# Optimization experiments

Measured on AMD Instinct MI355X. Metric: run time of the kernel, lower is better.

## Reference

```python
import jax, jax.numpy as jnp
import numpy as np
import functools

N, D, R, E, L, C, MAXDEG = 40000, 128, 3, 640000, 2, 40, 512
BN_EPS = 1e-5


def setup_inputs():
    ks = iter(jax.random.split(jax.random.key(0), 40))
    nrm = lambda s, sc=0.05: jax.random.normal(next(ks), s, dtype=jnp.float32) * sc
    x = jax.random.normal(next(ks), (N, D), dtype=jnp.float32)
    edge_indices = jax.random.randint(next(ks), (R, 2, E), 0, N, dtype=jnp.int32)
    out_emb = nrm((L, MAXDEG, D)).at[:, 0].set(0.0)  # padding_idx=0 -> zero row
    in_emb = nrm((L, MAXDEG, D)).at[:, 0].set(0.0)
    return dict(
        x=x, edge_indices=edge_indices,
        W_src=nrm((L, D, D)), b_src=nrm((L, D)),
        W_dst=nrm((L, D, D)), b_dst=nrm((L, D)),
        W_outf=nrm((L, D)), b_outf=nrm((L,)),
        W_inf=nrm((L, D)), b_inf=nrm((L,)),
        W_fc=nrm((L, D, D)), b_fc=nrm((L, D)),
        bn_gamma=jnp.ones((L, D), jnp.float32), bn_beta=jnp.zeros((L, D), jnp.float32),
        out_deg_emb=out_emb, in_deg_emb=in_emb,
        out_mask=jnp.ones((R, N), jnp.float32), out_mask_bias=jnp.zeros((R, N), jnp.float32),
        in_mask=jnp.ones((R, N), jnp.float32), in_mask_bias=jnp.zeros((R, N), jnp.float32),
        alpha=jnp.float32(0.5), tau=jnp.float32(0.0),
        W_lin=nrm((D, C)), b_lin=nrm((C,)),
    )


def _forward(x, W_src, b_src, W_dst, b_dst, W_outf, b_outf, W_inf, b_inf,
             W_fc, b_fc, bn_gamma, bn_beta, out_deg_emb, in_deg_emb,
             out_mask, out_mask_bias, in_mask, in_mask_bias, alpha, tau,
             W_lin, b_lin, edge_indices):
    seg = lambda d, i: jax.ops.segment_sum(d, i, num_segments=N)
    # source builds I with arange(0, N-1): identity with last diagonal entry missing
    i_mask = (jnp.arange(N) < N - 1).astype(jnp.float32)[:, None]

    rel = []
    for r in range(R):
        row, col = edge_indices[r, 0], edge_indices[r, 1]
        ones = jnp.ones(E, jnp.float32)
        out_deg, in_deg = seg(ones, row), seg(ones, col)
        ods = jnp.where(out_deg > 0, 1.0 / jnp.sqrt(jnp.maximum(out_deg, 1.0)), 0.0)
        ids_ = jnp.where(in_deg > 0, 1.0 / jnp.sqrt(jnp.maximum(in_deg, 1.0)), 0.0)
        # 'dir' norm: D_out^{-1/2} A D_in^{-1/2}; the transposed adj shares the same edge weights
        w = ods[row] * ids_[col]
        rel.append((row, col, w,
                    jnp.clip(out_deg, 0, MAXDEG - 1).astype(jnp.int32),
                    jnp.clip(in_deg, 0, MAXDEG - 1).astype(jnp.int32)))

    def spmm(r_, y):  # adj_norm @ y : gather cols, scatter-add to rows
        row, col, w = rel[r_][0], rel[r_][1], rel[r_][2]
        return seg(w[:, None] * y[col], row)

    def spmm_t(r_, y):  # adj_norm^T @ y
        row, col, w = rel[r_][0], rel[r_][1], rel[r_][2]
        return seg(w[:, None] * y[row], col)

    def dirichlet(mm, y):
        x1 = y / (jnp.sum(jnp.abs(y), axis=1, keepdims=True) + 1e-12)  # row_l1_normalize
        x1sq = x1 * x1
        return (i_mask * x1sq + mm(x1sq)) - 2.0 * ((i_mask * x1 + mm(x1)) * x1 - x1sq)

    eff_tau = jnp.exp(tau) + 0.1

    def conv(l, h):
        out = jnp.zeros((N, D), h.dtype)
        cis, cos_ = [], []
        for r in range(R):
            mm = functools.partial(spmm, r)
            mmt = functools.partial(spmm_t, r)
            out_nei, in_nei = mm(h), mmt(h)
            e_out, e_in = dirichlet(mm, h), dirichlet(mmt, h)
            c_out = (-e_out + out_deg_emb[l][rel[r][3]]) @ W_outf[l] + b_outf[l]  # [N]
            c_in = (-e_in + in_deg_emb[l][rel[r][4]]) @ W_inf[l] + b_inf[l]
            cm = jax.nn.softmax(jnp.stack([c_out, c_in], axis=1) / eff_tau, axis=1)  # tau_softmax
            c_out = cm[:, 0] * out_mask[r] + out_mask_bias[r]
            c_in = cm[:, 1] * in_mask[r] + in_mask_bias[r]
            out = out + c_out[:, None] * (out_nei @ W_src[l] + b_src[l]) \
                      + c_in[:, None] * (in_nei @ W_dst[l] + b_dst[l])
            cis.append(c_in)
            cos_.append(c_out)
        out = out / R
        # F.pad(x,(0,dim-x.shape[1])) is a no-op since input_dim == output_dim
        output = out + alpha * (h @ W_fc[l] + b_fc[l])
        mu, var = jnp.mean(output, axis=0), jnp.var(output, axis=0)  # BatchNorm1d (train mode)
        output = (output - mu) / jnp.sqrt(var + BN_EPS) * bn_gamma[l] + bn_beta[l]
        return output, jnp.mean(jnp.stack(cis), 0)[:, None], jnp.mean(jnp.stack(cos_), 0)[:, None]

    pos_h, neg_h = x, x
    pos_hs, neg_hs, gs, cins, couts = [], [], [], [], []
    for l in range(L):
        ph, ci, co = conv(l, pos_h)
        ph = jax.nn.relu(ph)  # jumping_knowledge truthy -> relu every layer; dropout p=0
        perm = jax.random.permutation(jax.random.key(100 + l), N)  # torch.randperm
        nh, _, _ = conv(l, neg_h[perm])
        nh = jax.nn.relu(nh)
        pos_h, neg_h = ph, nh
        pos_hs.append(ph)
        neg_hs.append(nh)
        gs.append(jnp.mean(ph, axis=0, keepdims=True))
        cins.append(ci)
        couts.append(co)
    c_ins = jnp.mean(jnp.stack(cins), 0)
    c_outs = jnp.mean(jnp.stack(couts), 0)
    jk = functools.reduce(jnp.maximum, pos_hs)  # JumpingKnowledge mode='max'
    logp = jax.nn.log_softmax(jk @ W_lin + b_lin, axis=1)
    return (logp, c_ins, c_outs, *pos_hs, *neg_hs, *gs)


def reference(x, edge_indices, W_src, b_src, W_dst, b_dst, W_outf, b_outf,
              W_inf, b_inf, W_fc, b_fc, bn_gamma, bn_beta, out_deg_emb,
              in_deg_emb, out_mask, out_mask_bias, in_mask, in_mask_bias,
              alpha, tau, W_lin, b_lin):
    return _forward(x, W_src, b_src, W_dst, b_dst, W_outf, b_outf, W_inf, b_inf,
                    W_fc, b_fc, bn_gamma, bn_beta, out_deg_emb, in_deg_emb,
                    out_mask, out_mask_bias, in_mask, in_mask_bias, alpha, tau,
                    W_lin, b_lin, edge_indices)
```

## Files before the change

### kernel.cpp

```cpp
#include <hip/hip_runtime.h>

constexpr int Nn = 40000;
constexpr int Dd = 128;
constexpr int Rr = 3;
constexpr int Ee = 640000;
constexpr int Ll = 2;
constexpr int Cc = 40;
constexpr int MAXD = 512;
constexpr float BN_EPS = 1e-5f;

constexpr int RB_ELEMS = 1024;
constexpr int RB_NB = (Nn + RB_ELEMS - 1) / RB_ELEMS;
constexpr int RB_BINS = 256;

constexpr int EB_ELEMS = 4096;
constexpr int EB_NB = (Ee + EB_ELEMS - 1) / EB_ELEMS;
constexpr int EB_H = 256 * EB_NB;

constexpr int HR_BINS = 13334;
constexpr int HR_PAD = 13344;
constexpr int HR_SB = 16;
constexpr int HR_CHUNK = (Ee + HR_SB - 1) / HR_SB;

__device__ __forceinline__ unsigned rotl32(unsigned x, int d) { return (x << d) | (x >> (32 - d)); }

__device__ void threefry2x32(unsigned k0, unsigned k1, unsigned c0, unsigned c1,
                             unsigned& o0, unsigned& o1) {
  unsigned ks2 = k0 ^ k1 ^ 0x1BD11BDAu;
  unsigned x0 = c0 + k0, x1 = c1 + k1;
#define TFR4(a,b,c,d2) \
  x0 += x1; x1 = rotl32(x1,a);  x1 ^= x0; \
  x0 += x1; x1 = rotl32(x1,b);  x1 ^= x0; \
  x0 += x1; x1 = rotl32(x1,c);  x1 ^= x0; \
  x0 += x1; x1 = rotl32(x1,d2); x1 ^= x0;
  TFR4(13,15,26,6);  x0 += k1;  x1 += ks2 + 1u;
  TFR4(17,29,16,24); x0 += ks2; x1 += k0 + 2u;
  TFR4(13,15,26,6);  x0 += k0;  x1 += k1 + 3u;
  TFR4(17,29,16,24); x0 += k1;  x1 += ks2 + 4u;
  TFR4(13,15,26,6);  x0 += ks2; x1 += k0 + 5u;
#undef TFR4
  o0 = x0; o1 = x1;
}

__global__ void k_genkeys(unsigned* __restrict__ keys, unsigned seed, int rounds,
                          int* __restrict__ vout, int doIota) {
  int i = blockIdx.x * blockDim.x + threadIdx.x;
  if (i >= Nn) return;
  unsigned k0 = 0u, k1 = seed, sk0 = 0u, sk1 = 0u;
  for (int rd = 0; rd < rounds; rd++) {
    unsigned a0, a1, b0, b1;
    threefry2x32(k0, k1, 0u, 0u, a0, a1);
    threefry2x32(k0, k1, 0u, 1u, b0, b1);
    sk0 = b0; sk1 = b1;
    k0 = a0; k1 = a1;
  }
  unsigned o0, o1;
  threefry2x32(sk0, sk1, 0u, (unsigned)i, o0, o1);
  keys[i] = o0 ^ o1;
  if (doIota) vout[i] = i;
}

__global__ void k_rhist(const unsigned* __restrict__ keys, int* __restrict__ hist, int shift) {
  __shared__ int lh[RB_BINS];
  int t = threadIdx.x;
  lh[t] = 0;
  __syncthreads();
  int base = blockIdx.x * RB_ELEMS;
  for (int i = t; i < RB_ELEMS; i += 256) {
    int g = base + i;
    if (g < Nn) atomicAdd(&lh[(keys[g] >> shift) & 255], 1);
  }
  __syncthreads();
  hist[t * RB_NB + blockIdx.x] = lh[t];
}

__device__ void scan_body(const int* cnt, int* off, int n, int items) {
  int t = threadIdx.x;
  int lo = t * items, hi = min(lo + items, n);
  int s = 0;
  for (int i = lo; i < hi; i++) s += cnt[i];
  int lane = t & 63, wid = t >> 6;
  int sc = s;
#pragma unroll
  for (int o = 1; o < 64; o <<= 1) {
    int v = __shfl_up(sc, o);
    if (lane >= o) sc += v;
  }
  __shared__ int wsum[16], woff[16];
  if (lane == 63) wsum[wid] = sc;
  __syncthreads();
  if (t == 0) {
    int a = 0;
    for (int w = 0; w < 16; w++) { woff[w] = a; a += wsum[w]; }
    off[n] = a;
  }
  __syncthreads();
  int run = woff[wid] + sc - s;
  for (int i = lo; i < hi; i++) {
    int v = cnt[i];
    off[i] = run;
    run += v;
  }
}

__global__ __launch_bounds__(1024) void k_scanN(const int* __restrict__ cnt, int* __restrict__ off,
                                                int n, int items) {
  scan_body(cnt, off, n, items);
}

__global__ __launch_bounds__(1024) void k_scan6(const int* __restrict__ odeg, const int* __restrict__ ideg,
                                                int* __restrict__ csr_off, int* __restrict__ csc_off) {
  int b = blockIdx.x;
  const int* cnt = (b < 3) ? (odeg + b * Nn) : (ideg + (b - 3) * Nn);
  int* off = (b < 3) ? (csr_off + b * (Nn + 1)) : (csc_off + (b - 3) * (Nn + 1));
  scan_body(cnt, off, Nn, (Nn + 1023) / 1024);
}

__global__ void k_rscatter(const unsigned* __restrict__ keys, const int* __restrict__ vals,
                           const int* __restrict__ scanned, int shift,
                           unsigned* __restrict__ okeys, int* __restrict__ ovals) {
  __shared__ int running[RB_BINS];
  __shared__ int wcount[4][RB_BINS];
  __shared__ int dbase[RB_BINS];
  int t = threadIdx.x;
  int lane = t & 63, w = t >> 6;
  running[t] = 0;
  dbase[t] = scanned[t * RB_NB + blockIdx.x];
  int base = blockIdx.x * RB_ELEMS;
  for (int rnd = 0; rnd < 4; rnd++) {
#pragma unroll
    for (int q = 0; q < 4; q++) wcount[q][t] = 0;
    __syncthreads();
    int g = base + rnd * 256 + t;
    bool valid = g < Nn;
    unsigned key = valid ? keys[g] : 0u;
    int d = (key >> shift) & 255;
    unsigned long long bb = __ballot(valid);
    unsigned long long mask = bb;
#pragma unroll
    for (int k = 0; k < 8; k++) {
      bool b = (d >> k) & 1;
      unsigned long long tt = __ballot(b && valid);
      mask &= b ? tt : ~tt;
    }
    mask &= bb;
    int riw = __popcll(mask & ((1ull << lane) - 1ull));
    int cnt_ = __popcll(mask);
    if (valid && riw == 0) wcount[w][d] = cnt_;
    __syncthreads();
    if (valid) {
      int prior = 0;
#pragma unroll
      for (int ww = 0; ww < 4; ww++) if (ww < w) prior += wcount[ww][d];
      int gp = dbase[d] + running[d] + prior + riw;
      okeys[gp] = key;
      ovals[gp] = vals[g];
    }
    __syncthreads();
    running[t] += wcount[0][t] + wcount[1][t] + wcount[2][t] + wcount[3][t];
    __syncthreads();
  }
}

__global__ void k_permrows(const float* __restrict__ src, const int* __restrict__ perm,
                           float* __restrict__ dst) {
  int row = blockIdx.x * 8 + (threadIdx.x >> 5);
  int lane = threadIdx.x & 31;
  if (row >= Nn) return;
  int p = perm[row];
  ((float4*)(dst + (size_t)row * Dd))[lane] = ((const float4*)(src + (size_t)p * Dd))[lane];
}

__global__ __launch_bounds__(256) void k_hist2(const int* __restrict__ ei, int* __restrict__ partials) {
  __shared__ int lh[HR_BINS];
  int bid = blockIdx.x;
  int sb = bid % HR_SB;
  int range = (bid / HR_SB) % 3;
  int j = bid / (3 * HR_SB);
  int rel = j >> 1, which = j & 1;
  const int* src = ei + (size_t)rel * 2 * Ee + (size_t)which * Ee;
  int lo = range * HR_BINS;
  for (int i = threadIdx.x; i < HR_BINS; i += 256) lh[i] = 0;
  __syncthreads();
  int e0 = sb * HR_CHUNK, e1 = min(e0 + HR_CHUNK, Ee);
  for (int e = e0 + threadIdx.x; e < e1; e += 256) {
    int v = src[e] - lo;
    if (v >= 0 && v < HR_BINS) atomicAdd(&lh[v], 1);
  }
  __syncthreads();
  int* dst = partials + (size_t)bid * HR_PAD;
  for (int i = threadIdx.x; i < HR_BINS; i += 256) dst[i] = lh[i];
}

__global__ void k_hreduce(const int* __restrict__ partials, int* __restrict__ odeg,
                          int* __restrict__ ideg) {
  int idx = blockIdx.x * 256 + threadIdx.x;
  if (idx >= 6 * Nn) return;
  int j = idx / Nn, bin = idx - j * Nn;
  int range = bin / HR_BINS, off = bin - range * HR_BINS;
  const int* p = partials + (size_t)((j * 3 + range) * HR_SB) * HR_PAD + off;
  int sum = 0;
#pragma unroll
  for (int b = 0; b < HR_SB; b++) sum += p[(size_t)b * HR_PAD];
  int rel = j >> 1;
  (j & 1 ? ideg : odeg)[rel * Nn + bin] = sum;
}

__global__ void k_degnorm(const int* __restrict__ odeg, const int* __restrict__ ideg,
                          float* __restrict__ ods, float* __restrict__ ids,
                          int* __restrict__ odix, int* __restrict__ idix) {
  int idx = blockIdx.x * blockDim.x + threadIdx.x;
  if (idx >= Rr * Nn) return;
  int od = odeg[idx], id_ = ideg[idx];
  ods[idx] = od > 0 ? 1.0f / sqrtf((float)od) : 0.0f;
  ids[idx] = id_ > 0 ? 1.0f / sqrtf((float)id_) : 0.0f;
  odix[idx] = od < MAXD - 1 ? od : MAXD - 1;
  idix[idx] = id_ < MAXD - 1 ? id_ : MAXD - 1;
}

__global__ void k_pack(const int* __restrict__ ei, unsigned* __restrict__ pcsr,
                       unsigned* __restrict__ pcsc) {
  int idx = blockIdx.x * 256 + threadIdx.x;
  if (idx >= 3 * Ee) return;
  int r = idx / Ee, e = idx - r * Ee;
  const int* base = ei + (size_t)r * 2 * Ee;
  unsigned rw = (unsigned)base[e], cl = (unsigned)base[Ee + e];
  pcsr[idx] = (rw << 16) | cl;
  pcsc[idx] = (cl << 16) | rw;
}

__global__ __launch_bounds__(256) void k_ehist(const unsigned* __restrict__ pin,
                                               int* __restrict__ hist, int shift) {
  __shared__ int lh[256];
  int a = blockIdx.x / EB_NB, blk = blockIdx.x % EB_NB;
  const unsigned* src = pin + (size_t)a * Ee;
  lh[threadIdx.x] = 0;
  __syncthreads();
  int base = blk * EB_ELEMS;
  for (int i = threadIdx.x; i < EB_ELEMS; i += 256) {
    int g = base + i;
    if (g < Ee) atomicAdd(&lh[(src[g] >> shift) & 255], 1);
  }
  __syncthreads();
  hist[(size_t)a * EB_H + threadIdx.x * EB_NB + blk] = lh[threadIdx.x];
}

__global__ __launch_bounds__(1024) void k_escan6(const int* __restrict__ hist, int* __restrict__ esc) {
  int a = blockIdx.x;
  scan_body(hist + (size_t)a * EB_H, esc + (size_t)a * (EB_H + 1), EB_H, (EB_H + 1023) / 1024);
}

__global__ __launch_bounds__(256) void k_escatter(const unsigned* __restrict__ pin,
                                                  const int* __restrict__ esc, int shift,
                                                  unsigned* __restrict__ pout) {
  __shared__ int running[256];
  __shared__ int wcount[4][256];
  __shared__ int dbase[256];
  int a = blockIdx.x / EB_NB, blk = blockIdx.x % EB_NB;
  const unsigned* src = pin + (size_t)a * Ee;
  unsigned* dst = pout + (size_t)a * Ee;
  int t = threadIdx.x;
  int lane = t & 63, w = t >> 6;
  running[t] = 0;
  dbase[t] = esc[(size_t)a * (EB_H + 1) + t * EB_NB + blk];
  int base = blk * EB_ELEMS;
  for (int rnd = 0; rnd < 16; rnd++) {
#pragma unroll
    for (int q = 0; q < 4; q++) wcount[q][t] = 0;
    __syncthreads();
    int g = base + rnd * 256 + t;
    bool valid = g < Ee;
    unsigned key = valid ? src[g] : 0u;
    int d = (key >> shift) & 255;
    unsigned long long bb = __ballot(valid);
    unsigned long long mask = bb;
#pragma unroll
    for (int k = 0; k < 8; k++) {
      bool b = (d >> k) & 1;
      unsigned long long tt = __ballot(b && valid);
      mask &= b ? tt : ~tt;
    }
    mask &= bb;
    int riw = __popcll(mask & ((1ull << lane) - 1ull));
    int cnt_ = __popcll(mask);
    if (valid && riw == 0) wcount[w][d] = cnt_;
    __syncthreads();
    if (valid) {
      int prior = 0;
#pragma unroll
      for (int ww = 0; ww < 4; ww++) if (ww < w) prior += wcount[ww][d];
      int gp = dbase[d] + running[d] + prior + riw;
      dst[gp] = key;
    }
    __syncthreads();
    running[t] += wcount[0][t] + wcount[1][t] + wcount[2][t] + wcount[3][t];
    __syncthreads();
  }
}

__global__ void k_rowscalar(const float* __restrict__ h, const float* __restrict__ Wfo,
                            const float* __restrict__ Wfi, float4* __restrict__ aux) {
  int wid = (blockIdx.x * blockDim.x + threadIdx.x) >> 6;
  int lane = threadIdx.x & 63;
  if (wid >= Nn) return;
  float2 a = ((const float2*)(h + (size_t)wid * Dd))[lane];
  float2 wo = ((const float2*)Wfo)[lane];
  float2 wi = ((const float2*)Wfi)[lane];
  float l1 = fabsf(a.x) + fabsf(a.y);
  float so = a.x * a.x * wo.x + a.y * a.y * wo.y;
  float si = a.x * a.x * wi.x + a.y * a.y * wi.y;
#pragma unroll
  for (int o = 32; o; o >>= 1) {
    l1 += __shfl_xor(l1, o);
    so += __shfl_xor(so, o);
    si += __shfl_xor(si, o);
  }
  if (lane == 0) {
    float ri = 1.0f / (l1 + 1e-12f);
    aux[wid] = make_float4(ri, ri * ri * so, ri * ri * si, 0.f);
  }
}

__global__ void k_lut(const float* __restrict__ eo, const float* __restrict__ ei_,
                      const float* __restrict__ Wfo, const float* __restrict__ Wfi,
                      float* __restrict__ luto, float* __restrict__ luti) {
  int wid = (blockIdx.x * blockDim.x + threadIdx.x) >> 6;
  int lane = threadIdx.x & 63;
  if (wid >= MAXD) return;
  float2 a = ((const float2*)(eo + (size_t)wid * Dd))[lane];
  float2 b = ((const float2*)(ei_ + (size_t)wid * Dd))[lane];
  float2 wo = ((const float2*)Wfo)[lane];
  float2 wi = ((const float2*)Wfi)[lane];
  float so = a.x * wo.x + a.y * wo.y;
  float si = b.x * wi.x + b.y * wi.y;
#pragma unroll
  for (int o = 32; o; o >>= 1) { so += __shfl_xor(so, o); si += __shfl_xor(si, o); }
  if (lane == 0) { luto[wid] = so; luti[wid] = si; }
}

__global__ __launch_bounds__(512) void k_csrdir3(
    const int* __restrict__ csr_off, const unsigned* __restrict__ pcsr,
    const int* __restrict__ csc_off, const unsigned* __restrict__ pcsc,
    const float* __restrict__ ods_r, const float* __restrict__ ids_r,
    const float4* __restrict__ aux, const float* __restrict__ h,
    const float* __restrict__ Wfo, const float* __restrict__ Wfi,
    const float* __restrict__ luto, const float* __restrict__ luti,
    const int* __restrict__ odix, const int* __restrict__ idix,
    const float* __restrict__ bo, const float* __restrict__ bi,
    const float* __restrict__ taup,
    const float* __restrict__ omask, const float* __restrict__ omaskb,
    const float* __restrict__ imask, const float* __restrict__ imaskb,
    float* __restrict__ Tout, float* __restrict__ Tin,
    float* __restrict__ sco, float* __restrict__ sci,
    float* __restrict__ co_acc, float* __restrict__ ci_acc,
    int first, int is_pos) {
  __shared__ float lq[8], lp[8], lc[8];
  int t = threadIdx.x;
  int wv = t >> 6, lane = t & 63;
  int dir = wv >> 2;
  int n = blockIdx.x * 4 + (wv & 3);
  const int* off = dir ? csc_off : csr_off;
  const unsigned* nbrp = dir ? pcsc : pcsr;
  const float* scn = dir ? ods_r : ids_r;
  float a_self = (dir ? ids_r : ods_r)[n];
  const float* Wf = dir ? Wfi : Wfo;
  int s0 = off[n], s1 = off[n + 1];
  int hl = lane & 31, half = lane >> 5;
  float4 wf4 = ((const float4*)Wf)[hl];
  float4 hn4 = ((const float4*)(h + (size_t)n * Dd))[hl];
  float rn = aux[n].x;
  float4 s = make_float4(0.f, 0.f, 0.f, 0.f);
  float4 pa = make_float4(0.f, 0.f, 0.f, 0.f);
  float qacc = 0.f;
  for (int base = s0; base < s1; base += 64) {
    int eidx = base + lane;
    bool valid = eidx < s1;
    int mi = valid ? (int)(nbrp[eidx] & 0xFFFFu) : 0;
    float4 av = valid ? aux[mi] : make_float4(0.f, 0.f, 0.f, 0.f);
    float scv = valid ? scn[mi] : 0.f;
    float qsel = dir ? av.z : av.y;
    int cnt = min(64, s1 - base);
#pragma unroll 4
    for (int j = half; j < cnt; j += 2) {
      int m = __shfl(mi, j);
      float sc = __shfl(scv, j);
      float rm = __shfl(av.x, j);
      float qv = __shfl(qsel, j);
      float w = a_self * sc;
      float wrm = w * rm;
      float4 hv = ((const float4*)(h + (size_t)m * Dd))[hl];
      s.x += w * hv.x; s.y += w * hv.y; s.z += w * hv.z; s.w += w * hv.w;
      pa.x += wrm * hv.x; pa.y += wrm * hv.y; pa.z += wrm * hv.z; pa.w += wrm * hv.w;
      qacc += w * qv;
    }
  }
  s.x += __shfl_xor(s.x, 32); s.y += __shfl_xor(s.y, 32);
  s.z += __shfl_xor(s.z, 32); s.w += __shfl_xor(s.w, 32);
  pa.x += __shfl_xor(pa.x, 32); pa.y += __shfl_xor(pa.y, 32);
  pa.z += __shfl_xor(pa.z, 32); pa.w += __shfl_xor(pa.w, 32);
  qacc += __shfl_xor(qacc, 32);
  float pd = rn * (hn4.x * wf4.x * pa.x + hn4.y * wf4.y * pa.y +
                   hn4.z * wf4.z * pa.z + hn4.w * wf4.w * pa.w);
#pragma unroll
  for (int o = 16; o; o >>= 1) pd += __shfl_xor(pd, o);
  if (lane == 0) { lq[wv] = qacc; lp[wv] = pd; }
  __syncthreads();
  if (t < 4) {
    int nn = blockIdx.x * 4 + t;
    float Qo_ = lq[t], Po_ = lp[t], Qi_ = lq[4 + t], Pi_ = lp[4 + t];
    float4 a2 = aux[nn];
    float im = (nn < Nn - 1) ? 1.0f : 0.0f;
    float so_ = luto[odix[nn]] + bo[0] - (Qo_ - 2.0f * Po_ + (2.0f - im) * a2.y);
    float si_ = luti[idix[nn]] + bi[0] - (Qi_ - 2.0f * Pi_ + (2.0f - im) * a2.z);
    float tt = expf(taup[0]) + 0.1f;
    float aa = so_ / tt, bb = si_ / tt;
    float mm = fmaxf(aa, bb);
    float ea = expf(aa - mm), eb = expf(bb - mm);
    float inv = 1.0f / (ea + eb);
    float co = ea * inv * omask[nn] + omaskb[nn];
    float ci = eb * inv * imask[nn] + imaskb[nn];
    lc[t] = co; lc[4 + t] = ci;
    if (first) { sco[nn] = co; sci[nn] = ci; }
    else       { sco[nn] += co; sci[nn] += ci; }
    if (is_pos) { co_acc[nn] += co; ci_acc[nn] += ci; }
  }
  __syncthreads();
  float c = lc[wv];
  if (lane < 32) {
    float* T = dir ? Tin : Tout;
    size_t o = (size_t)n * Dd;
    float4 v = make_float4(c * s.x, c * s.y, c * s.z, c * s.w);
    if (!first) {
      float4 old = ((const float4*)(T + o))[hl];
      v.x += old.x; v.y += old.y; v.z += old.z; v.w += old.w;
    }
    ((float4*)(T + o))[hl] = v;
  }
}

__global__ __launch_bounds__(256) void k_gemmconv(
    const float* __restrict__ Tout, const float* __restrict__ Tin, const float* __restrict__ h,
    const float* __restrict__ Wsrc, const float* __restrict__ Wdst, const float* __restrict__ Wfc,
    const float* __restrict__ bsrc, const float* __restrict__ bdst, const float* __restrict__ bfc,
    const float* __restrict__ sco, const float* __restrict__ sci,
    const float* __restrict__ alphap, float* __restrict__ pre, float* __restrict__ bnsum) {
  __shared__ float Asm[64][36];
  __shared__ float Bsm[32][132];
  __shared__ float lsum[128], lsum2[128];
  int t = threadIdx.x;
  int rg = t >> 5, cg = t & 31;
  int m0 = blockIdx.x * 64;
  int arow = t >> 2, aq = t & 3;
  float alpha = alphap[0];
  float acc[8][4];
#pragma unroll
  for (int r = 0; r < 8; r++)
#pragma unroll
    for (int c = 0; c < 4; c++) acc[r][c] = 0.f;
  for (int kt = 0; kt < 12; kt++) {
    int sec = kt >> 2, kc = (kt & 3) * 32;
    const float* Ap = sec == 0 ? Tout : (sec == 1 ? Tin : h);
    const float* Wp = sec == 0 ? Wsrc : (sec == 1 ? Wdst : Wfc);
    float sA = (sec == 2) ? alpha : (1.0f / (float)Rr);
    __syncthreads();
    {
      const float4* src = (const float4*)(Ap + (size_t)(m0 + arow) * Dd + kc + aq * 8);
      float4 v0 = src[0], v1 = src[1];
      float4* d0 = (float4*)&Asm[arow][aq * 8];
      d0[0] = make_float4(v0.x * sA, v0.y * sA, v0.z * sA, v0.w * sA);
      d0[1] = make_float4(v1.x * sA, v1.y * sA, v1.z * sA, v1.w * sA);
    }
#pragma unroll
    for (int j = 0; j < 4; j++) {
      int idx = t + j * 256;
      int k = idx >> 5, d4 = idx & 31;
      *(float4*)&Bsm[k][d4 * 4] = *(const float4*)(Wp + (size_t)(kc + k) * Dd + d4 * 4);
    }
    __syncthreads();
#pragma unroll
    for (int kk = 0; kk < 32; kk += 4) {
      float4 af[8], bf[4];
#pragma unroll
      for (int r = 0; r < 8; r++) af[r] = *(const float4*)&Asm[rg * 8 + r][kk];
#pragma unroll
      for (int j = 0; j < 4; j++) bf[j] = *(const float4*)&Bsm[kk + j][cg * 4];
#pragma unroll
      for (int r = 0; r < 8; r++) {
        const float* ap = (const float*)&af[r];
#pragma unroll
        for (int j = 0; j < 4; j++) {
          const float* bp = (const float*)&bf[j];
          acc[r][0] += ap[j] * bp[0];
          acc[r][1] += ap[j] * bp[1];
          acc[r][2] += ap[j] * bp[2];
          acc[r][3] += ap[j] * bp[3];
        }
      }
    }
  }
  float4 vb1 = *(const float4*)(bsrc + cg * 4);
  float4 vb2 = *(const float4*)(bdst + cg * 4);
  float4 vbf = *(const float4*)(bfc + cg * 4);
  float ps[4] = {0.f, 0.f, 0.f, 0.f}, ps2[4] = {0.f, 0.f, 0.f, 0.f};
#pragma unroll
  for (int r = 0; r < 8; r++) {
    int row = m0 + rg * 8 + r;
    size_t o = (size_t)row * Dd + cg * 4;
    float s1 = sco[row] * (1.0f / (float)Rr), s2 = sci[row] * (1.0f / (float)Rr);
    float4 v;
    v.x = acc[r][0] + s1 * vb1.x + s2 * vb2.x + alpha * vbf.x;
    v.y = acc[r][1] + s1 * vb1.y + s2 * vb2.y + alpha * vbf.y;
    v.z = acc[r][2] + s1 * vb1.z + s2 * vb2.z + alpha * vbf.z;
    v.w = acc[r][3] + s1 * vb1.w + s2 * vb2.w + alpha * vbf.w;
    *(float4*)(pre + o) = v;
    ps[0] += v.x; ps[1] += v.y; ps[2] += v.z; ps[3] += v.w;
    ps2[0] += v.x * v.x; ps2[1] += v.y * v.y; ps2[2] += v.z * v.z; ps2[3] += v.w * v.w;
  }
  if (t < 128) { lsum[t] = 0.f; lsum2[t] = 0.f; }
  __syncthreads();
#pragma unroll
  for (int j = 0; j < 4; j++) {
    atomicAdd(&lsum[cg * 4 + j], ps[j]);
    atomicAdd(&lsum2[cg * 4 + j], ps2[j]);
  }
  __syncthreads();
  if (t < 128) atomicAdd(&bnsum[t], lsum[t]);
  else if (t < 256) atomicAdd(&bnsum[t], lsum2[t - 128]);
}

__global__ void k_bnapply(const float* __restrict__ pre, const float* __restrict__ sums,
                          const float* __restrict__ gamma, const float* __restrict__ beta,
                          float* __restrict__ hout, float* __restrict__ gs, int do_gs) {
  __shared__ float ls[256];
  int c = threadIdx.x & 127, sub = threadIdx.x >> 7;
  float mu = sums[c] * (1.0f / (float)Nn);
  float var = sums[c + 128] * (1.0f / (float)Nn) - mu * mu;
  float sc = gamma[c] / sqrtf(var + BN_EPS);
  float bt = beta[c];
  float g = 0.f;
  for (int n = blockIdx.x * 2 + sub; n < Nn; n += gridDim.x * 2) {
    float v = (pre[(size_t)n * Dd + c] - mu) * sc + bt;
    v = fmaxf(v, 0.f);
    hout[(size_t)n * Dd + c] = v;
    g += v;
  }
  if (do_gs) {
    ls[threadIdx.x] = g;
    __syncthreads();
    if (sub == 0) atomicAdd(&gs[c], (ls[c] + ls[c + 128]) * (1.0f / (float)Nn));
  }
}

__global__ void k_cio(const float* __restrict__ ci_acc, const float* __restrict__ co_acc,
                      float* __restrict__ cins, float* __restrict__ couts) {
  int n = blockIdx.x * blockDim.x + threadIdx.x;
  if (n < Nn) {
    cins[n] = ci_acc[n] * (1.0f / (float)(Ll * Rr));
    couts[n] = co_acc[n] * (1.0f / (float)(Ll * Rr));
  }
}

__global__ __launch_bounds__(64) void k_logp(const float* __restrict__ ph0, const float* __restrict__ ph1,
                      const float* __restrict__ Wlin, const float* __restrict__ blin,
                      float* __restrict__ logp) {
  __shared__ float jk[Dd];
  __shared__ float lg[Cc];
  int n = blockIdx.x, t = threadIdx.x;
  for (int d = t; d < Dd; d += 64) jk[d] = fmaxf(ph0[(size_t)n * Dd + d], ph1[(size_t)n * Dd + d]);
  __syncthreads();
  if (t < Cc) {
    float acc = blin[t];
    for (int k = 0; k < Dd; k++) acc += jk[k] * Wlin[k * Cc + t];
    lg[t] = acc;
  }
  __syncthreads();
  float m = -1e30f;
  for (int c = 0; c < Cc; c++) m = fmaxf(m, lg[c]);
  float s = 0.f;
  for (int c = 0; c < Cc; c++) s += expf(lg[c] - m);
  float lse = m + logf(s);
  if (t < Cc) logp[(size_t)n * Cc + t] = lg[t] - lse;
}

extern "C" void kernel_launch(void* const* d_in, const int* in_sizes, int n_in,
                              void* d_out, int out_size, void* d_ws, size_t ws_size,
                              hipStream_t stream) {
  const float* x      = (const float*)d_in[0];
  const int*   ei     = (const int*)d_in[1];
  const float* W_src  = (const float*)d_in[2];
  const float* b_src  = (const float*)d_in[3];
  const float* W_dst  = (const float*)d_in[4];
  const float* b_dst  = (const float*)d_in[5];
  const float* W_outf = (const float*)d_in[6];
  const float* b_outf = (const float*)d_in[7];
  const float* W_inf  = (const float*)d_in[8];
  const float* b_inf  = (const float*)d_in[9];
  const float* W_fc   = (const float*)d_in[10];
  const float* b_fc   = (const float*)d_in[11];
  const float* gamma  = (const float*)d_in[12];
  const float* beta   = (const float*)d_in[13];
  const float* oemb   = (const float*)d_in[14];
  const float* iemb   = (const float*)d_in[15];
  const float* omask  = (const float*)d_in[16];
  const float* omaskb = (const float*)d_in[17];
  const float* imask  = (const float*)d_in[18];
  const float* imaskb = (const float*)d_in[19];
  const float* alphap = (const float*)d_in[20];
  const float* taup   = (const float*)d_in[21];
  const float* Wlin   = (const float*)d_in[22];
  const float* blin   = (const float*)d_in[23];

  float* out   = (float*)d_out;
  float* logp  = out;
  float* cins  = logp + (size_t)Nn * Cc;
  float* couts = cins + Nn;
  float* ph0   = couts + Nn;
  float* ph1   = ph0 + (size_t)Nn * Dd;
  float* nh0   = ph1 + (size_t)Nn * Dd;
  float* nh1   = nh0 + (size_t)Nn * Dd;
  float* gs0   = nh1 + (size_t)Nn * Dd;
  float* gs1   = gs0 + Dd;

  char* p = (char*)d_ws;
  auto alloc = [&](size_t bytes) -> void* {
    void* q = (void*)p;
    p += (bytes + 255) & ~(size_t)255;
    return q;
  };
  float* pre   = (float*)alloc((size_t)Nn * Dd * 4);
  float* Tout  = (float*)alloc((size_t)Nn * Dd * 4);
  float* Tin   = (float*)alloc((size_t)Nn * Dd * 4);
  float* hperm = (float*)alloc((size_t)Nn * Dd * 4);
  unsigned* pbuf = (unsigned*)alloc((size_t)6 * Ee * 4);
  size_t qwords = (size_t)6 * Ee;
  size_t pwords = (size_t)(6 * 3 * HR_SB) * HR_PAD;
  unsigned* qbuf = (unsigned*)alloc((qwords > pwords ? qwords : pwords) * 4);
  int* partials = (int*)qbuf;
  int* csr_off = (int*)alloc((size_t)Rr * (Nn + 1) * 4);
  int* csc_off = (int*)alloc((size_t)Rr * (Nn + 1) * 4);
  int* odeg    = (int*)alloc((size_t)Rr * Nn * 4);
  int* ideg    = (int*)alloc((size_t)Rr * Nn * 4);
  float* ods   = (float*)alloc((size_t)Rr * Nn * 4);
  float* ids   = (float*)alloc((size_t)Rr * Nn * 4);
  int* odix    = (int*)alloc((size_t)Rr * Nn * 4);
  int* idix    = (int*)alloc((size_t)Rr * Nn * 4);
  float4* aux  = (float4*)alloc((size_t)Nn * 16);
  float* sco   = (float*)alloc((size_t)Nn * 4 * 2);
  float* sci   = sco + Nn;
  float* coacc = (float*)alloc((size_t)Nn * 4 * 2);
  float* ciacc = coacc + Nn;
  float* luto  = (float*)alloc(MAXD * 4);
  float* luti  = (float*)alloc(MAXD * 4);
  float* bnsum = (float*)alloc(256 * 4);
  unsigned* kbuf0 = (unsigned*)alloc((size_t)Nn * 4);
  unsigned* kbuf1 = (unsigned*)alloc((size_t)Nn * 4);
  int* vbuf0 = (int*)alloc((size_t)Nn * 4);
  int* vbuf1 = (int*)alloc((size_t)Nn * 4);
  int* rhist = (int*)alloc((size_t)(RB_BINS * RB_NB + 1) * 4);
  int* rscan = (int*)alloc((size_t)(RB_BINS * RB_NB + 1) * 4);
  int* ehist = (int*)alloc((size_t)6 * EB_H * 4);
  int* escan = (int*)alloc((size_t)6 * (EB_H + 1) * 4);

  k_hist2<<<6 * 3 * HR_SB, 256, 0, stream>>>(ei, partials);
  k_hreduce<<<(6 * Nn + 255) / 256, 256, 0, stream>>>(partials, odeg, ideg);
  k_degnorm<<<(Rr * Nn + 255) / 256, 256, 0, stream>>>(odeg, ideg, ods, ids, odix, idix);
  k_scan6<<<6, 1024, 0, stream>>>(odeg, ideg, csr_off, csc_off);
  k_pack<<<(3 * Ee + 255) / 256, 256, 0, stream>>>(ei, pbuf, pbuf + (size_t)3 * Ee);
  k_ehist<<<6 * EB_NB, 256, 0, stream>>>(pbuf, ehist, 16);
  k_escan6<<<6, 1024, 0, stream>>>(ehist, escan);
  k_escatter<<<6 * EB_NB, 256, 0, stream>>>(pbuf, escan, 16, qbuf);
  k_ehist<<<6 * EB_NB, 256, 0, stream>>>(qbuf, ehist, 24);
  k_escan6<<<6, 1024, 0, stream>>>(ehist, escan);
  k_escatter<<<6 * EB_NB, 256, 0, stream>>>(qbuf, escan, 24, pbuf);
  hipMemsetAsync(coacc, 0, (size_t)Nn * 4 * 2, stream);

  auto radix4 = [&]() {
    for (int pass = 0; pass < 4; pass++) {
      const unsigned* ik = (pass & 1) ? kbuf1 : kbuf0;
      const int*      iv = (pass & 1) ? vbuf1 : vbuf0;
      unsigned*       ok = (pass & 1) ? kbuf0 : kbuf1;
      int*            ov = (pass & 1) ? vbuf0 : vbuf1;
      int shift = pass * 8;
      k_rhist<<<RB_NB, 256, 0, stream>>>(ik, rhist, shift);
      k_scanN<<<1, 1024, 0, stream>>>(rhist, rscan, RB_BINS * RB_NB, (RB_BINS * RB_NB + 1023) / 1024);
      k_rscatter<<<RB_NB, 256, 0, stream>>>(ik, iv, rscan, shift, ok, ov);
    }
  };

  auto make_perm = [&](unsigned seed) {
    k_genkeys<<<(Nn + 255) / 256, 256, 0, stream>>>(kbuf0, seed, 1, vbuf0, 1);
    radix4();
    k_genkeys<<<(Nn + 255) / 256, 256, 0, stream>>>(kbuf0, seed, 2, vbuf0, 0);
    radix4();
  };

  auto conv = [&](int l, const float* hin, float* hout, float* gs, int is_pos) {
    const float* Wfo = W_outf + l * Dd;
    const float* Wfi = W_inf + l * Dd;
    k_rowscalar<<<Nn / 4, 256, 0, stream>>>(hin, Wfo, Wfi, aux);
    for (int r = 0; r < Rr; r++) {
      k_csrdir3<<<Nn / 4, 512, 0, stream>>>(csr_off + r * (Nn + 1), pbuf + (size_t)r * Ee,
                                            csc_off + r * (Nn + 1), pbuf + (size_t)(3 + r) * Ee,
                                            ods + r * Nn, ids + r * Nn, aux, hin, Wfo, Wfi,
                                            luto, luti, odix + r * Nn, idix + r * Nn,
                                            b_outf + l, b_inf + l, taup,
                                            omask + (size_t)r * Nn, omaskb + (size_t)r * Nn,
                                            imask + (size_t)r * Nn, imaskb + (size_t)r * Nn,
                                            Tout, Tin, sco, sci, coacc, ciacc,
                                            r == 0 ? 1 : 0, is_pos);
    }
    hipMemsetAsync(bnsum, 0, 256 * 4, stream);
    k_gemmconv<<<Nn / 64, 256, 0, stream>>>(Tout, Tin, hin,
                                            W_src + (size_t)l * Dd * Dd, W_dst + (size_t)l * Dd * Dd,
                                            W_fc + (size_t)l * Dd * Dd,
                                            b_src + l * Dd, b_dst + l * Dd, b_fc + l * Dd,
                                            sco, sci, alphap, pre, bnsum);
    if (is_pos) hipMemsetAsync(gs, 0, Dd * 4, stream);
    k_bnapply<<<256, 256, 0, stream>>>(pre, bnsum, gamma + l * Dd, beta + l * Dd, hout, gs, is_pos);
  };

  k_lut<<<MAXD / 4, 256, 0, stream>>>(oemb, iemb, W_outf, W_inf, luto, luti);
  conv(0, x, ph0, gs0, 1);
  make_perm(100u);
  k_permrows<<<Nn / 8, 256, 0, stream>>>(x, vbuf0, hperm);
  conv(0, hperm, nh0, nullptr, 0);

  k_lut<<<MAXD / 4, 256, 0, stream>>>(oemb + (size_t)MAXD * Dd, iemb + (size_t)MAXD * Dd,
                                      W_outf + Dd, W_inf + Dd, luto, luti);
  conv(1, ph0, ph1, gs1, 1);
  make_perm(101u);
  k_permrows<<<Nn / 8, 256, 0, stream>>>(nh0, vbuf0, hperm);
  conv(1, hperm, nh1, nullptr, 0);

  k_cio<<<(Nn + 255) / 256, 256, 0, stream>>>(ciacc, coacc, cins, couts);
  k_logp<<<Nn, 64, 0, stream>>>(ph0, ph1, Wlin, blin, logp);
}
```

Before: 2.440 ms.

## Batch both permutation sorts together and shrink csrdir3 blocks

Generates the random keys for both layer permutations in one launch and runs the two radix sorts as a batched pass. This halves the number of small sort kernel launches, since a 40k-element sort is dominated by launch overhead and single-block scans. It also cuts k_csrdir3 blocks from 512 to 256 threads (2 nodes per block instead of 4) and folds k_cio into k_logp to remove one more launch. The cost is double-sized sort buffers and a different occupancy profile for the edge gather kernel.

```diff
diff --git a/kernel.cpp b/kernel.cpp
--- a/kernel.cpp
+++ b/kernel.cpp
@@ -12,6 +12,7 @@
 constexpr int RB_ELEMS = 1024;
 constexpr int RB_NB = (Nn + RB_ELEMS - 1) / RB_ELEMS;
 constexpr int RB_BINS = 256;
+constexpr int RB_H = RB_BINS * RB_NB;
 
 constexpr int EB_ELEMS = 4096;
 constexpr int EB_NB = (Ee + EB_ELEMS - 1) / EB_ELEMS;
@@ -42,10 +43,12 @@
   o0 = x0; o1 = x1;
 }
 
-__global__ void k_genkeys(unsigned* __restrict__ keys, unsigned seed, int rounds,
-                          int* __restrict__ vout, int doIota) {
+__global__ void k_genkeys2(unsigned* __restrict__ keys, unsigned seed0, unsigned seed1,
+                           int rounds, int* __restrict__ vout, int doIota) {
   int i = blockIdx.x * blockDim.x + threadIdx.x;
-  if (i >= Nn) return;
+  if (i >= 2 * Nn) return;
+  int seg = i / Nn, li = i - seg * Nn;
+  unsigned seed = seg ? seed1 : seed0;
   unsigned k0 = 0u, k1 = seed, sk0 = 0u, sk1 = 0u;
   for (int rd = 0; rd < rounds; rd++) {
     unsigned a0, a1, b0, b1;
@@ -55,23 +58,25 @@
     k0 = a0; k1 = a1;
   }
   unsigned o0, o1;
-  threefry2x32(sk0, sk1, 0u, (unsigned)i, o0, o1);
+  threefry2x32(sk0, sk1, 0u, (unsigned)li, o0, o1);
   keys[i] = o0 ^ o1;
-  if (doIota) vout[i] = i;
-}
-
-__global__ void k_rhist(const unsigned* __restrict__ keys, int* __restrict__ hist, int shift) {
+  if (doIota) vout[i] = li;
+}
+
+__global__ void k_rhist2(const unsigned* __restrict__ keys, int* __restrict__ hist, int shift) {
   __shared__ int lh[RB_BINS];
+  int a = blockIdx.x / RB_NB, blk = blockIdx.x % RB_NB;
+  const unsigned* src = keys + (size_t)a * Nn;
   int t = threadIdx.x;
   lh[t] = 0;
   __syncthreads();
-  int base = blockIdx.x * RB_ELEMS;
+  int base = blk * RB_ELEMS;
   for (int i = t; i < RB_ELEMS; i += 256) {
     int g = base + i;
-    if (g < Nn) atomicAdd(&lh[(keys[g] >> shift) & 255], 1);
-  }
-  __syncthreads();
-  hist[t * RB_NB + blockIdx.x] = lh[t];
+    if (g < Nn) atomicAdd(&lh[(src[g] >> shift) & 255], 1);
+  }
+  __syncthreads();
+  hist[(size_t)a * RB_H + t * RB_NB + blk] = lh[t];
 }
 
 __device__ void scan_body(const int* cnt, int* off, int n, int items) {
@@ -103,9 +108,9 @@
   }
 }
 
-__global__ __launch_bounds__(1024) void k_scanN(const int* __restrict__ cnt, int* __restrict__ off,
-                                                int n, int items) {
-  scan_body(cnt, off, n, items);
+__global__ __launch_bounds__(1024) void k_scanP(const int* __restrict__ hist, int* __restrict__ esc) {
+  int a = blockIdx.x;
+  scan_body(hist + (size_t)a * RB_H, esc + (size_t)a * (RB_H + 1), RB_H, (RB_H + 1023) / 1024);
 }
 
 __global__ __launch_bounds__(1024) void k_scan6(const int* __restrict__ odeg, const int* __restrict__ ideg,
@@ -116,24 +121,29 @@
   scan_body(cnt, off, Nn, (Nn + 1023) / 1024);
 }
 
-__global__ void k_rscatter(const unsigned* __restrict__ keys, const int* __restrict__ vals,
-                           const int* __restrict__ scanned, int shift,
-                           unsigned* __restrict__ okeys, int* __restrict__ ovals) {
+__global__ void k_rscatter2(const unsigned* __restrict__ keys, const int* __restrict__ vals,
+                            const int* __restrict__ scanned, int shift,
+                            unsigned* __restrict__ okeys, int* __restrict__ ovals) {
   __shared__ int running[RB_BINS];
   __shared__ int wcount[4][RB_BINS];
   __shared__ int dbase[RB_BINS];
+  int a = blockIdx.x / RB_NB, blk = blockIdx.x % RB_NB;
+  const unsigned* ksrc = keys + (size_t)a * Nn;
+  const int* vsrc = vals + (size_t)a * Nn;
+  unsigned* kdst = okeys + (size_t)a * Nn;
+  int* vdst = ovals + (size_t)a * Nn;
   int t = threadIdx.x;
   int lane = t & 63, w = t >> 6;
   running[t] = 0;
-  dbase[t] = scanned[t * RB_NB + blockIdx.x];
-  int base = blockIdx.x * RB_ELEMS;
+  dbase[t] = scanned[(size_t)a * (RB_H + 1) + t * RB_NB + blk];
+  int base = blk * RB_ELEMS;
   for (int rnd = 0; rnd < 4; rnd++) {
 #pragma unroll
     for (int q = 0; q < 4; q++) wcount[q][t] = 0;
     __syncthreads();
     int g = base + rnd * 256 + t;
     bool valid = g < Nn;
-    unsigned key = valid ? keys[g] : 0u;
+    unsigned key = valid ? ksrc[g] : 0u;
     int d = (key >> shift) & 255;
     unsigned long long bb = __ballot(valid);
     unsigned long long mask = bb;
@@ -153,8 +163,8 @@
 #pragma unroll
       for (int ww = 0; ww < 4; ww++) if (ww < w) prior += wcount[ww][d];
       int gp = dbase[d] + running[d] + prior + riw;
-      okeys[gp] = key;
-      ovals[gp] = vals[g];
+      kdst[gp] = key;
+      vdst[gp] = vsrc[g];
     }
     __syncthreads();
     running[t] += wcount[0][t] + wcount[1][t] + wcount[2][t] + wcount[3][t];
@@ -338,7 +348,7 @@
   if (lane == 0) { luto[wid] = so; luti[wid] = si; }
 }
 
-__global__ __launch_bounds__(512) void k_csrdir3(
+__global__ __launch_bounds__(256) void k_csrdir3(
     const int* __restrict__ csr_off, const unsigned* __restrict__ pcsr,
     const int* __restrict__ csc_off, const unsigned* __restrict__ pcsc,
     const float* __restrict__ ods_r, const float* __restrict__ ids_r,
@@ -354,11 +364,11 @@
     float* __restrict__ sco, float* __restrict__ sci,
     float* __restrict__ co_acc, float* __restrict__ ci_acc,
     int first, int is_pos) {
-  __shared__ float lq[8], lp[8], lc[8];
+  __shared__ float lq[4], lp[4], lc[4];
   int t = threadIdx.x;
   int wv = t >> 6, lane = t & 63;
-  int dir = wv >> 2;
-  int n = blockIdx.x * 4 + (wv & 3);
+  int dir = wv >> 1;
+  int n = blockIdx.x * 2 + (wv & 1);
   const int* off = dir ? csc_off : csr_off;
   const unsigned* nbrp = dir ? pcsc : pcsr;
   const float* scn = dir ? ods_r : ids_r;
@@ -405,9 +415,9 @@
   for (int o = 16; o; o >>= 1) pd += __shfl_xor(pd, o);
   if (lane == 0) { lq[wv] = qacc; lp[wv] = pd; }
   __syncthreads();
-  if (t < 4) {
-    int nn = blockIdx.x * 4 + t;
-    float Qo_ = lq[t], Po_ = lp[t], Qi_ = lq[4 + t], Pi_ = lp[4 + t];
+  if (t < 2) {
+    int nn = blockIdx.x * 2 + t;
+    float Qo_ = lq[t], Po_ = lp[t], Qi_ = lq[2 + t], Pi_ = lp[2 + t];
     float4 a2 = aux[nn];
     float im = (nn < Nn - 1) ? 1.0f : 0.0f;
     float so_ = luto[odix[nn]] + bo[0] - (Qo_ - 2.0f * Po_ + (2.0f - im) * a2.y);
@@ -419,7 +429,7 @@
     float inv = 1.0f / (ea + eb);
     float co = ea * inv * omask[nn] + omaskb[nn];
     float ci = eb * inv * imask[nn] + imaskb[nn];
-    lc[t] = co; lc[4 + t] = ci;
+    lc[t] = co; lc[2 + t] = ci;
     if (first) { sco[nn] = co; sci[nn] = ci; }
     else       { sco[nn] += co; sci[nn] += ci; }
     if (is_pos) { co_acc[nn] += co; ci_acc[nn] += ci; }
@@ -551,21 +561,18 @@
   }
 }
 
-__global__ void k_cio(const float* __restrict__ ci_acc, const float* __restrict__ co_acc,
-                      float* __restrict__ cins, float* __restrict__ couts) {
-  int n = blockIdx.x * blockDim.x + threadIdx.x;
-  if (n < Nn) {
-    cins[n] = ci_acc[n] * (1.0f / (float)(Ll * Rr));
-    couts[n] = co_acc[n] * (1.0f / (float)(Ll * Rr));
-  }
-}
-
 __global__ __launch_bounds__(64) void k_logp(const float* __restrict__ ph0, const float* __restrict__ ph1,
                       const float* __restrict__ Wlin, const float* __restrict__ blin,
+                      const float* __restrict__ ci_acc, const float* __restrict__ co_acc,
+                      float* __restrict__ cins, float* __restrict__ couts,
                       float* __restrict__ logp) {
   __shared__ float jk[Dd];
   __shared__ float lg[Cc];
   int n = blockIdx.x, t = threadIdx.x;
+  if (t == 63) {
+    cins[n] = ci_acc[n] * (1.0f / (float)(Ll * Rr));
+    couts[n] = co_acc[n] * (1.0f / (float)(Ll * Rr));
+  }
   for (int d = t; d < Dd; d += 64) jk[d] = fmaxf(ph0[(size_t)n * Dd + d], ph1[(size_t)n * Dd + d]);
   __syncthreads();
   if (t < Cc) {
@@ -652,12 +659,12 @@
   float* luto  = (float*)alloc(MAXD * 4);
   float* luti  = (float*)alloc(MAXD * 4);
   float* bnsum = (float*)alloc(256 * 4);
-  unsigned* kbuf0 = (unsigned*)alloc((size_t)Nn * 4);
-  unsigned* kbuf1 = (unsigned*)alloc((size_t)Nn * 4);
-  int* vbuf0 = (int*)alloc((size_t)Nn * 4);
-  int* vbuf1 = (int*)alloc((size_t)Nn * 4);
-  int* rhist = (int*)alloc((size_t)(RB_BINS * RB_NB + 1) * 4);
-  int* rscan = (int*)alloc((size_t)(RB_BINS * RB_NB + 1) * 4);
+  unsigned* kbuf0 = (unsigned*)alloc((size_t)2 * Nn * 4);
+  unsigned* kbuf1 = (unsigned*)alloc((size_t)2 * Nn * 4);
+  int* vbuf0 = (int*)alloc((size_t)2 * Nn * 4);
+  int* vbuf1 = (int*)alloc((size_t)2 * Nn * 4);
+  int* rhist = (int*)alloc((size_t)2 * (RB_H + 1) * 4);
+  int* rscan = (int*)alloc((size_t)2 * (RB_H + 1) * 4);
   int* ehist = (int*)alloc((size_t)6 * EB_H * 4);
   int* escan = (int*)alloc((size_t)6 * (EB_H + 1) * 4);
 
@@ -674,32 +681,29 @@
   k_escatter<<<6 * EB_NB, 256, 0, stream>>>(qbuf, escan, 24, pbuf);
   hipMemsetAsync(coacc, 0, (size_t)Nn * 4 * 2, stream);
 
-  auto radix4 = [&]() {
+  auto radix4b = [&]() {
     for (int pass = 0; pass < 4; pass++) {
       const unsigned* ik = (pass & 1) ? kbuf1 : kbuf0;
       const int*      iv = (pass & 1) ? vbuf1 : vbuf0;
       unsigned*       ok = (pass & 1) ? kbuf0 : kbuf1;
       int*            ov = (pass & 1) ? vbuf0 : vbuf1;
       int shift = pass * 8;
-      k_rhist<<<RB_NB, 256, 0, stream>>>(ik, rhist, shift);
-      k_scanN<<<1, 1024, 0, stream>>>(rhist, rscan, RB_BINS * RB_NB, (RB_BINS * RB_NB + 1023) / 1024);
-      k_rscatter<<<RB_NB, 256, 0, stream>>>(ik, iv, rscan, shift, ok, ov);
+      k_rhist2<<<2 * RB_NB, 256, 0, stream>>>(ik, rhist, shift);
+      k_scanP<<<2, 1024, 0, stream>>>(rhist, rscan);
+      k_rscatter2<<<2 * RB_NB, 256, 0, stream>>>(ik, iv, rscan, shift, ok, ov);
     }
   };
-
-  auto make_perm = [&](unsigned seed) {
-    k_genkeys<<<(Nn + 255) / 256, 256, 0, stream>>>(kbuf0, seed, 1, vbuf0, 1);
-    radix4();
-    k_genkeys<<<(Nn + 255) / 256, 256, 0, stream>>>(kbuf0, seed, 2, vbuf0, 0);
-    radix4();
-  };
+  k_genkeys2<<<(2 * Nn + 255) / 256, 256, 0, stream>>>(kbuf0, 100u, 101u, 1, vbuf0, 1);
+  radix4b();
+  k_genkeys2<<<(2 * Nn + 255) / 256, 256, 0, stream>>>(kbuf0, 100u, 101u, 2, vbuf0, 0);
+  radix4b();
 
   auto conv = [&](int l, const float* hin, float* hout, float* gs, int is_pos) {
     const float* Wfo = W_outf + l * Dd;
     const float* Wfi = W_inf + l * Dd;
     k_rowscalar<<<Nn / 4, 256, 0, stream>>>(hin, Wfo, Wfi, aux);
     for (int r = 0; r < Rr; r++) {
-      k_csrdir3<<<Nn / 4, 512, 0, stream>>>(csr_off + r * (Nn + 1), pbuf + (size_t)r * Ee,
+      k_csrdir3<<<Nn / 2, 256, 0, stream>>>(csr_off + r * (Nn + 1), pbuf + (size_t)r * Ee,
                                             csc_off + r * (Nn + 1), pbuf + (size_t)(3 + r) * Ee,
                                             ods + r * Nn, ids + r * Nn, aux, hin, Wfo, Wfi,
                                             luto, luti, odix + r * Nn, idix + r * Nn,
@@ -721,17 +725,14 @@
 
   k_lut<<<MAXD / 4, 256, 0, stream>>>(oemb, iemb, W_outf, W_inf, luto, luti);
   conv(0, x, ph0, gs0, 1);
-  make_perm(100u);
   k_permrows<<<Nn / 8, 256, 0, stream>>>(x, vbuf0, hperm);
   conv(0, hperm, nh0, nullptr, 0);
 
   k_lut<<<MAXD / 4, 256, 0, stream>>>(oemb + (size_t)MAXD * Dd, iemb + (size_t)MAXD * Dd,
                                       W_outf + Dd, W_inf + Dd, luto, luti);
   conv(1, ph0, ph1, gs1, 1);
-  make_perm(101u);
-  k_permrows<<<Nn / 8, 256, 0, stream>>>(nh0, vbuf0, hperm);
+  k_permrows<<<Nn / 8, 256, 0, stream>>>(nh0, vbuf0 + Nn, hperm);
   conv(1, hperm, nh1, nullptr, 0);
 
-  k_cio<<<(Nn + 255) / 256, 256, 0, stream>>>(ciacc, coacc, cins, couts);
-  k_logp<<<Nn, 64, 0, stream>>>(ph0, ph1, Wlin, blin, logp);
-}
+  k_logp<<<Nn, 64, 0, stream>>>(ph0, ph1, Wlin, blin, ciacc, coacc, cins, couts, logp);
+}
```

Measured after the change: 2.232 ms. -8.5%, faster.
